# Kernel tuning notes

Measured on AMD Instinct MI355X. Metric: run time of the kernel, lower is better.

## Reference

```python
import jax, jax.numpy as jnp
import numpy as np

N_NODES = 100000
N_EDGES = 1600000
N_GRAPHS = 2000
F_IN = 16
HEADS = 8
C = 16            # per-head out channels (hidden_dim)
HC = HEADS * C    # 128
N_CLASSES = 2
NEG_SLOPE = 0.2   # PyG GATConv default leaky_relu slope


def setup_inputs() -> dict:
    key = jax.random.key(0)
    ks = jax.random.split(key, 12)
    x = jax.random.normal(ks[0], (N_NODES, F_IN), dtype=jnp.float32)
    edge_index = jax.random.randint(ks[1], (2, N_EDGES), 0, N_NODES, dtype=jnp.int32)
    batch = jnp.sort(jax.random.randint(ks[2], (N_NODES,), 0, N_GRAPHS, dtype=jnp.int32))
    s1 = 1.0 / np.sqrt(F_IN)
    s2 = 1.0 / np.sqrt(HC)
    return {
        "x": x,
        "edge_index": edge_index,
        "batch": batch,
        "W1": jax.random.normal(ks[3], (F_IN, HC), dtype=jnp.float32) * s1,
        "a1_src": jax.random.normal(ks[4], (HEADS, C), dtype=jnp.float32) * s2,
        "a1_dst": jax.random.normal(ks[5], (HEADS, C), dtype=jnp.float32) * s2,
        "b1": jnp.zeros((HC,), dtype=jnp.float32),
        "W2": jax.random.normal(ks[6], (HC, HC), dtype=jnp.float32) * s2,
        "a2_src": jax.random.normal(ks[7], (HEADS, C), dtype=jnp.float32) * s2,
        "a2_dst": jax.random.normal(ks[8], (HEADS, C), dtype=jnp.float32) * s2,
        "b2": jnp.zeros((HC,), dtype=jnp.float32),
        "lin_W": jax.random.normal(ks[9], (HC, N_CLASSES), dtype=jnp.float32) * s2,
        "lin_b": jnp.zeros((N_CLASSES,), dtype=jnp.float32),
    }


def gat_layer(h_in, src, dst, W, a_src, a_dst, b, num_nodes):
    # h: [N, H, C] per-head transformed features
    h = (h_in @ W).reshape(num_nodes, HEADS, C)
    # per-node attention half-logits: [N, H]
    logit_src = jnp.einsum('nhc,hc->nh', h, a_src)
    logit_dst = jnp.einsum('nhc,hc->nh', h, a_dst)
    # per-edge logits [E, H]
    e = jax.nn.leaky_relu(logit_src[src] + logit_dst[dst], NEG_SLOPE)
    # segment softmax over incoming edges of each destination node
    m = jax.ops.segment_max(e, dst, num_segments=num_nodes)
    m = jnp.where(jnp.isfinite(m), m, 0.0)
    ex = jnp.exp(e - m[dst])
    denom = jax.ops.segment_sum(ex, dst, num_segments=num_nodes)
    alpha = ex / jnp.maximum(denom[dst], 1e-16)
    # weighted scatter-add aggregation: [N, H, C]
    out = jax.ops.segment_sum(alpha[:, :, None] * h[src], dst, num_segments=num_nodes)
    return out.reshape(num_nodes, HC) + b


def reference(x, edge_index, batch, W1, a1_src, a1_dst, b1, W2, a2_src, a2_dst, b2, lin_W, lin_b):
    n = x.shape[0]
    # PyG GATConv adds self-loops by default
    loops = jnp.arange(n, dtype=edge_index.dtype)
    src = jnp.concatenate([edge_index[0], loops])
    dst = jnp.concatenate([edge_index[1], loops])
    h = jax.nn.relu(gat_layer(x, src, dst, W1, a1_src, a1_dst, b1, n))
    h = jax.nn.relu(gat_layer(h, src, dst, W2, a2_src, a2_dst, b2, n))
    # global mean pool per graph
    sums = jax.ops.segment_sum(h, batch, num_segments=N_GRAPHS)
    counts = jax.ops.segment_sum(jnp.ones((n, 1), h.dtype), batch, num_segments=N_GRAPHS)
    pooled = sums / jnp.maximum(counts, 1.0)
    logits = pooled @ lin_W + lin_b
    return jax.nn.softmax(logits, axis=1)
```

## Files before the change

### kernel.cpp

```cpp
#include <hip/hip_runtime.h>
#include <math.h>

#define N_NODES 100000
#define N_EDGESI 1600000
#define E_TOTAL (N_EDGESI + N_NODES)
#define N_GRAPHS 2000
#define F_IN 16
#define HEADS 8
#define CPH 16
#define HC 128
#define NEG 0.2f

#define BSHIFT 9
#define BNODES (1<<BSHIFT)
#define NBUK ((N_NODES + BNODES - 1)/BNODES)
#define BCAP 12288
#define BIN_EPT 32
#define BIN_TPB 256
#define BIN_EPB (BIN_EPT*BIN_TPB)
#define NBIN_BLK ((E_TOTAL + BIN_EPB - 1)/BIN_EPB)

#define GOFF_BLK ((N_NODES+255)/256)
#define WCONV_BLK ((HC*HC)/256)
#define XCONV_BLK ((N_NODES*4 + 255)/256)
#define W1CONV_BLK ((HC*32)/256)

typedef __bf16 bf16x8 __attribute__((ext_vector_type(8)));
typedef float  f32x4  __attribute__((ext_vector_type(4)));

__device__ __forceinline__ float leaky(float x){ return fmaxf(x, NEG*x); }
__device__ __forceinline__ float bf2f(unsigned short u){ return __uint_as_float(((unsigned)u)<<16); }
__device__ __forceinline__ unsigned short f2bf(float f){
  unsigned u = __float_as_uint(f);
  unsigned r = (u + 0x7fffu + ((u>>16)&1u)) >> 16;
  return (unsigned short)r;
}
__device__ __forceinline__ float blo(unsigned u){ return __uint_as_float(u<<16); }
__device__ __forceinline__ float bhi(unsigned u){ return __uint_as_float(u & 0xffff0000u); }

__global__ void k_pre(const int* __restrict__ ei, int* __restrict__ gpos, unsigned* __restrict__ gbin,
                      const int* __restrict__ batch, int* __restrict__ goff,
                      const float* __restrict__ W2, unsigned short* __restrict__ w2t,
                      const float* __restrict__ x, unsigned short* __restrict__ xbf,
                      const float* __restrict__ W1, unsigned short* __restrict__ w1t){
  int blk = blockIdx.x;
  if (blk < NBIN_BLK){
    __shared__ int cnt[NBUK];
    __shared__ int rnk[NBUK];
    __shared__ int bbase[NBUK];
    int t = threadIdx.x;
    for (int i = t; i < NBUK; i += BIN_TPB){ cnt[i] = 0; rnk[i] = 0; }
    __syncthreads();
    int base = blk*BIN_EPB;
    #pragma unroll 4
    for (int i = 0; i < BIN_EPT; ++i){
      int e = base + i*BIN_TPB + t;
      if (e < E_TOTAL){
        unsigned d = (e < N_EDGESI) ? (unsigned)ei[N_EDGESI + e] : (unsigned)(e - N_EDGESI);
        atomicAdd(&cnt[d >> BSHIFT], 1);
      }
    }
    __syncthreads();
    for (int i = t; i < NBUK; i += BIN_TPB){
      int v = cnt[i];
      bbase[i] = v ? atomicAdd(&gpos[i], v) : 0;
    }
    __syncthreads();
    #pragma unroll 4
    for (int i = 0; i < BIN_EPT; ++i){
      int e = base + i*BIN_TPB + t;
      if (e < E_TOTAL){
        unsigned s, d;
        if (e < N_EDGESI){ s = (unsigned)ei[e]; d = (unsigned)ei[N_EDGESI + e]; }
        else { s = d = (unsigned)(e - N_EDGESI); }
        int b = (int)(d >> BSHIFT);
        int r = atomicAdd(&rnk[b], 1);
        gbin[(size_t)b*BCAP + bbase[b] + r] = ((d & (BNODES-1u)) << 17) | s;
      }
    }
  } else if (blk < NBIN_BLK + GOFF_BLK){
    int n = (blk - NBIN_BLK)*256 + threadIdx.x;
    if (n >= N_NODES) return;
    int b = batch[n];
    if (n == 0){ for (int g = 0; g <= b; ++g) goff[g] = 0; }
    int b1 = (n+1 < N_NODES) ? batch[n+1] : N_GRAPHS;
    for (int g = b+1; g <= b1; ++g) goff[g] = n+1;
  } else if (blk < NBIN_BLK + GOFF_BLK + WCONV_BLK){
    int i = (blk - NBIN_BLK - GOFF_BLK)*256 + threadIdx.x;
    if (i >= HC*HC) return;
    int c = i >> 7, k = i & 127;
    w2t[i] = f2bf(W2[k*HC + c]);
  } else if (blk < NBIN_BLK + GOFF_BLK + WCONV_BLK + XCONV_BLK){
    int p = (blk - NBIN_BLK - GOFF_BLK - WCONV_BLK)*256 + threadIdx.x;
    if (p >= N_NODES*4) return;
    int n = p >> 2, q = p & 3;
    float4 xv = ((const float4*)(x + n*F_IN))[q];
    ushort4 o; o.x = f2bf(xv.x); o.y = f2bf(xv.y); o.z = f2bf(xv.z); o.w = f2bf(xv.w);
    ((ushort4*)(xbf + (size_t)n*32))[q] = o;
    ushort4 z; z.x = 0; z.y = 0; z.z = 0; z.w = 0;
    ((ushort4*)(xbf + (size_t)n*32 + 16))[q] = z;
  } else {
    int i = (blk - NBIN_BLK - GOFF_BLK - WCONV_BLK - XCONV_BLK)*256 + threadIdx.x;
    if (i >= HC*32) return;
    int c = i >> 5, k = i & 31;
    w1t[i] = (k < F_IN) ? f2bf(W1[k*HC + c]) : (unsigned short)0;
  }
}

__global__ __launch_bounds__(512) void k_csr(
                      const int* __restrict__ gpos, const unsigned* __restrict__ gbin,
                      int* __restrict__ off, int* __restrict__ csrc){
  __shared__ int lcnt[BNODES];
  __shared__ int wsum[8];
  __shared__ int gp[NBUK];
  __shared__ int sbase;
  int b = blockIdx.x, t = threadIdx.x;
  for (int i = t; i < NBUK; i += 512) gp[i] = gpos[i];
  lcnt[t] = 0;
  __syncthreads();
  if (t == 0){ int s = 0; for (int j = 0; j < b; ++j) s += gp[j]; sbase = s; }
  int nb = gp[b];
  const unsigned* bb = gbin + (size_t)b*BCAP;
  __syncthreads();
  int base = sbase;
  for (int i = t; i < nb; i += 512) atomicAdd(&lcnt[bb[i] >> 17], 1);
  __syncthreads();
  int lane = t & 63, wv = t >> 6;
  int v = lcnt[t];
  int sc = v;
  #pragma unroll
  for (int o = 1; o < 64; o <<= 1){ int u = __shfl_up(sc, o, 64); if (lane >= o) sc += u; }
  if (lane == 63) wsum[wv] = sc;
  __syncthreads();
  if (wv == 0 && lane < 8){
    int w2 = wsum[lane];
    #pragma unroll
    for (int o = 1; o < 8; o <<= 1){ int u = __shfl_up(w2, o, 64); if (lane >= o) w2 += u; }
    wsum[lane] = w2;
  }
  __syncthreads();
  int excl = (wv ? wsum[wv-1] : 0) + sc - v;
  int d = (b << BSHIFT) + t;
  if (d < N_NODES) off[d] = base + excl;
  if (b == NBUK-1 && t == 0) off[N_NODES] = E_TOTAL;
  __syncthreads();
  lcnt[t] = base + excl;
  __syncthreads();
  for (int i = t; i < nb; i += 512){
    unsigned en = bb[i];
    int p = atomicAdd(&lcnt[en >> 17], 1);
    csrc[p] = (int)(en & 0x1ffffu);
  }
}

template<int KS>
__global__ __launch_bounds__(256) void k_gemm_mfma(
                             const unsigned short* __restrict__ hin,
                             const unsigned short* __restrict__ wt,
                             const float* __restrict__ asrc, const float* __restrict__ adst,
                             unsigned short* __restrict__ hb,
                             float* __restrict__ ls, float* __restrict__ ld){
  __shared__ unsigned short hls[64][132];
  const int KST = KS*32;
  int t = threadIdx.x, lane = t & 63, wv = t >> 6;
  int n0 = blockIdx.x*64 + wv*16;
  int rowl = lane & 15, kgrp = lane >> 4;
  int row = n0 + rowl;
  int rowc = (row < N_NODES) ? row : (N_NODES-1);
  bf16x8 a[KS];
  #pragma unroll
  for (int ks = 0; ks < KS; ++ks)
    a[ks] = *(const bf16x8*)(hin + (size_t)rowc*KST + ks*32 + kgrp*8);
  #pragma unroll
  for (int ct = 0; ct < 8; ++ct){
    f32x4 acc = {0.f, 0.f, 0.f, 0.f};
    int col = ct*16 + rowl;
    #pragma unroll
    for (int ks = 0; ks < KS; ++ks){
      bf16x8 b = *(const bf16x8*)(wt + (size_t)col*KST + ks*32 + kgrp*8);
      acc = __builtin_amdgcn_mfma_f32_16x16x32_bf16(a[ks], b, acc, 0, 0, 0);
    }
    #pragma unroll
    for (int r = 0; r < 4; ++r){
      int lrow = wv*16 + kgrp*4 + r;
      int ro = n0 + kgrp*4 + r;
      unsigned short hv = f2bf(acc[r]);
      hls[lrow][col] = hv;
      if (ro < N_NODES) hb[(size_t)ro*HC + col] = hv;
    }
  }
  __syncthreads();
  #pragma unroll
  for (int pp = 0; pp < 2; ++pp){
    int p = t + pp*256;
    int lrow = p >> 3, h = p & 7;
    int gn = blockIdx.x*64 + lrow;
    if (gn < N_NODES){
      const unsigned short* rp = &hls[lrow][h*16];
      uint2 A = *(const uint2*)rp;
      uint2 B = *(const uint2*)(rp+4);
      uint2 C = *(const uint2*)(rp+8);
      uint2 D = *(const uint2*)(rp+12);
      float c[16] = { blo(A.x), bhi(A.x), blo(A.y), bhi(A.y),
                      blo(B.x), bhi(B.x), blo(B.y), bhi(B.y),
                      blo(C.x), bhi(C.x), blo(C.y), bhi(C.y),
                      blo(D.x), bhi(D.x), blo(D.y), bhi(D.y) };
      const float* as = asrc + h*CPH;
      const float* ad = adst + h*CPH;
      float s0 = 0.f, s1 = 0.f;
      #pragma unroll
      for (int q = 0; q < 16; ++q){ s0 += c[q]*as[q]; s1 += c[q]*ad[q]; }
      ls[gn*8 + h] = s0;
      ld[gn*8 + h] = s1;
    }
  }
}

__global__ void k_agg(const int* __restrict__ off, const int* __restrict__ csrc,
                      const unsigned short* __restrict__ hb, const float* __restrict__ ls,
                      const float* __restrict__ ld, const float* __restrict__ bias,
                      unsigned short* __restrict__ outb){
  int wid = threadIdx.x >> 6, lane = threadIdx.x & 63;
  int n = blockIdx.x*4 + wid;
  if (n >= N_NODES) return;
  int rs = __builtin_amdgcn_readfirstlane(off[n]);
  int re = __builtin_amdgcn_readfirstlane(off[n+1]);
  int q = lane >> 4;
  int l = lane & 15;
  int h = l >> 1;
  float ldh = ld[n*8 + h];
  const uint4* hb4 = (const uint4*)hb;
  float ac0=0.f, ac1=0.f, ac2=0.f, ac3=0.f, ac4=0.f, ac5=0.f, ac6=0.f, ac7=0.f, dsum=0.f;
  #define AGG_BODY(J) { \
    int s = __shfl(sv, (J), 64); \
    float g = ls[s*8 + h]; \
    float ex = __expf(leaky(g + ldh)); \
    uint4 v = hb4[(size_t)s*16 + l]; \
    ac0 += ex*blo(v.x); ac1 += ex*bhi(v.x); \
    ac2 += ex*blo(v.y); ac3 += ex*bhi(v.y); \
    ac4 += ex*blo(v.z); ac5 += ex*bhi(v.z); \
    ac6 += ex*blo(v.w); ac7 += ex*bhi(v.w); \
    dsum += ex; }
  int nb = re - rs;
  for (int cb = 0; cb < nb; cb += 64){
    int cnt = nb - cb; if (cnt > 64) cnt = 64;
    int sv = csrc[rs + cb + (lane < cnt ? lane : 0)];
    int jj = 0;
    for (; jj + 16 <= cnt; jj += 16){
      AGG_BODY(jj+q) AGG_BODY(jj+q+4) AGG_BODY(jj+q+8) AGG_BODY(jj+q+12)
    }
    for (int j = jj + q; j < cnt; j += 4) AGG_BODY(j)
  }
  #undef AGG_BODY
  ac0 += __shfl_xor(ac0,16,64); ac0 += __shfl_xor(ac0,32,64);
  ac1 += __shfl_xor(ac1,16,64); ac1 += __shfl_xor(ac1,32,64);
  ac2 += __shfl_xor(ac2,16,64); ac2 += __shfl_xor(ac2,32,64);
  ac3 += __shfl_xor(ac3,16,64); ac3 += __shfl_xor(ac3,32,64);
  ac4 += __shfl_xor(ac4,16,64); ac4 += __shfl_xor(ac4,32,64);
  ac5 += __shfl_xor(ac5,16,64); ac5 += __shfl_xor(ac5,32,64);
  ac6 += __shfl_xor(ac6,16,64); ac6 += __shfl_xor(ac6,32,64);
  ac7 += __shfl_xor(ac7,16,64); ac7 += __shfl_xor(ac7,32,64);
  dsum += __shfl_xor(dsum,16,64); dsum += __shfl_xor(dsum,32,64);
  if (q == 0){
    float inv = 1.f/fmaxf(dsum, 1e-16f);
    float4 b0 = ((const float4*)bias)[l*2];
    float4 b1 = ((const float4*)bias)[l*2+1];
    uint4 o;
    o.x = (unsigned)f2bf(fmaxf(ac0*inv + b0.x, 0.f)) | ((unsigned)f2bf(fmaxf(ac1*inv + b0.y, 0.f)) << 16);
    o.y = (unsigned)f2bf(fmaxf(ac2*inv + b0.z, 0.f)) | ((unsigned)f2bf(fmaxf(ac3*inv + b0.w, 0.f)) << 16);
    o.z = (unsigned)f2bf(fmaxf(ac4*inv + b1.x, 0.f)) | ((unsigned)f2bf(fmaxf(ac5*inv + b1.y, 0.f)) << 16);
    o.w = (unsigned)f2bf(fmaxf(ac6*inv + b1.z, 0.f)) | ((unsigned)f2bf(fmaxf(ac7*inv + b1.w, 0.f)) << 16);
    ((uint4*)outb)[(size_t)n*16 + l] = o;
  }
}

__global__ void k_poolcls(const unsigned short* __restrict__ h, const int* __restrict__ goff,
                          const float* __restrict__ lw, const float* __restrict__ lb,
                          float* __restrict__ out){
  __shared__ float sh[4][HC];
  int g = blockIdx.x;
  int t = threadIdx.x, lane = t & 63, wv = t >> 6;
  int s = goff[g], epos = goff[g+1];
  float a0 = 0.f, a1 = 0.f;
  const ushort2* h2 = (const ushort2*)h;
  for (int n = s + wv; n < epos; n += 4){
    ushort2 v = h2[(size_t)n*64 + lane];
    a0 += bf2f(v.x); a1 += bf2f(v.y);
  }
  sh[wv][lane*2] = a0; sh[wv][lane*2+1] = a1;
  __syncthreads();
  if (wv == 0){
    int c0 = lane*2;
    float p0 = sh[0][c0] + sh[1][c0] + sh[2][c0] + sh[3][c0];
    float p1 = sh[0][c0+1] + sh[1][c0+1] + sh[2][c0+1] + sh[3][c0+1];
    int cntg = epos - s;
    float invc = 1.f/fmaxf((float)cntg, 1.f);
    float v0 = p0*invc, v1 = p1*invc;
    float l0 = v0*lw[c0*2+0] + v1*lw[(c0+1)*2+0];
    float l1 = v0*lw[c0*2+1] + v1*lw[(c0+1)*2+1];
    #pragma unroll
    for (int o = 32; o >= 1; o >>= 1){ l0 += __shfl_xor(l0,o,64); l1 += __shfl_xor(l1,o,64); }
    if (lane == 0){
      l0 += lb[0]; l1 += lb[1];
      float m = fmaxf(l0,l1);
      float e0 = __expf(l0-m), e1 = __expf(l1-m);
      float si = e0 + e1;
      out[g*2]   = e0/si;
      out[g*2+1] = e1/si;
    }
  }
}

extern "C" void kernel_launch(void* const* d_in, const int* in_sizes, int n_in,
                              void* d_out, int out_size, void* d_ws, size_t ws_size,
                              hipStream_t stream){
  const float* x   = (const float*)d_in[0];
  const int*   ei  = (const int*)d_in[1];
  const int*   bat = (const int*)d_in[2];
  const float* W1  = (const float*)d_in[3];
  const float* a1s = (const float*)d_in[4];
  const float* a1d = (const float*)d_in[5];
  const float* b1  = (const float*)d_in[6];
  const float* W2  = (const float*)d_in[7];
  const float* a2s = (const float*)d_in[8];
  const float* a2d = (const float*)d_in[9];
  const float* b2  = (const float*)d_in[10];
  const float* lw  = (const float*)d_in[11];
  const float* lb  = (const float*)d_in[12];
  float* out = (float*)d_out;

  char* w = (char*)d_ws;
  auto alloc = [&](size_t bytes)->void*{ void* p = (void*)w; w += (bytes + 511) & ~size_t(511); return p; };
  int* off    = (int*)alloc((size_t)(N_NODES+1)*4);
  int* csrc   = (int*)alloc((size_t)E_TOTAL*4);
  int* goff   = (int*)alloc((size_t)(N_GRAPHS+1)*4);
  int* gpos   = (int*)alloc((size_t)NBUK*4);
  unsigned* gbin = (unsigned*)alloc((size_t)NBUK*BCAP*4);
  unsigned short* w2t  = (unsigned short*)alloc((size_t)HC*HC*2);
  unsigned short* w1t  = (unsigned short*)alloc((size_t)HC*32*2);
  unsigned short* xbf  = (unsigned short*)alloc((size_t)N_NODES*32*2);
  unsigned short* hbf  = (unsigned short*)alloc((size_t)N_NODES*HC*2);
  unsigned short* hbf2 = (unsigned short*)alloc((size_t)N_NODES*HC*2);
  float* lsb  = (float*)alloc((size_t)N_NODES*HEADS*4);
  float* ldb  = (float*)alloc((size_t)N_NODES*HEADS*4);

  hipMemsetAsync(gpos, 0, (size_t)NBUK*4, stream);

  k_pre  <<<NBIN_BLK + GOFF_BLK + WCONV_BLK + XCONV_BLK + W1CONV_BLK,BIN_TPB,0,stream>>>(
           ei, gpos, gbin, bat, goff, W2, w2t, x, xbf, W1, w1t);
  k_gemm_mfma<1><<<(N_NODES+63)/64,256,0,stream>>>(xbf, w1t, a1s, a1d, hbf, lsb, ldb);
  k_csr  <<<NBUK,512,0,stream>>>(gpos, gbin, off, csrc);

  k_agg  <<<(N_NODES+3)/4,256,0,stream>>>(off, csrc, hbf, lsb, ldb, b1, hbf2);
  k_gemm_mfma<4><<<(N_NODES+63)/64,256,0,stream>>>(hbf2, w2t, a2s, a2d, hbf, lsb, ldb);
  k_agg  <<<(N_NODES+3)/4,256,0,stream>>>(off, csrc, hbf, lsb, ldb, b2, hbf2);

  k_poolcls<<<N_GRAPHS,256,0,stream>>>(hbf2, goff, lw, lb, out);
}
```

Measured before the change: 274.9 us.

## Replace per-bucket CSR build with global degree scan and split scatter

New measurement: 371.1 us. 35.0% more time.

```diff
diff --git a/kernel.cpp b/kernel.cpp
--- a/kernel.cpp
+++ b/kernel.cpp
@@ -10,6 +10,8 @@
 #define CPH 16
 #define HC 128
 #define NEG 0.2f
+#define SCAN_B 1024
+#define NB_SCAN ((N_NODES + SCAN_B - 1)/SCAN_B)
 
 #define BSHIFT 9
 #define BNODES (1<<BSHIFT)
@@ -19,6 +21,7 @@
 #define BIN_TPB 256
 #define BIN_EPB (BIN_EPT*BIN_TPB)
 #define NBIN_BLK ((E_TOTAL + BIN_EPB - 1)/BIN_EPB)
+#define CSR_SPLIT 8
 
 #define GOFF_BLK ((N_NODES+255)/256)
 #define WCONV_BLK ((HC*HC)/256)
@@ -39,6 +42,7 @@
 __device__ __forceinline__ float bhi(unsigned u){ return __uint_as_float(u & 0xffff0000u); }
 
 __global__ void k_pre(const int* __restrict__ ei, int* __restrict__ gpos, unsigned* __restrict__ gbin,
+                      int* __restrict__ cnt_g,
                       const int* __restrict__ batch, int* __restrict__ goff,
                       const float* __restrict__ W2, unsigned short* __restrict__ w2t,
                       const float* __restrict__ x, unsigned short* __restrict__ xbf,
@@ -58,6 +62,7 @@
       if (e < E_TOTAL){
         unsigned d = (e < N_EDGESI) ? (unsigned)ei[N_EDGESI + e] : (unsigned)(e - N_EDGESI);
         atomicAdd(&cnt[d >> BSHIFT], 1);
+        atomicAdd(&cnt_g[d], 1);
       }
     }
     __syncthreads();
@@ -107,48 +112,72 @@
   }
 }
 
-__global__ __launch_bounds__(512) void k_csr(
-                      const int* __restrict__ gpos, const unsigned* __restrict__ gbin,
-                      int* __restrict__ off, int* __restrict__ csrc){
-  __shared__ int lcnt[BNODES];
-  __shared__ int wsum[8];
-  __shared__ int gp[NBUK];
-  __shared__ int sbase;
-  int b = blockIdx.x, t = threadIdx.x;
-  for (int i = t; i < NBUK; i += 512) gp[i] = gpos[i];
-  lcnt[t] = 0;
-  __syncthreads();
-  if (t == 0){ int s = 0; for (int j = 0; j < b; ++j) s += gp[j]; sbase = s; }
-  int nb = gp[b];
+__global__ void k_scan1(const int* __restrict__ cnt, int* __restrict__ off, int* __restrict__ bsum){
+  __shared__ int ws[16];
+  int b = blockIdx.x, t = threadIdx.x, lane = t & 63, wv = t >> 6;
+  int i = b*SCAN_B + t;
+  int v = (i < N_NODES) ? cnt[i] : 0;
+  int sc = v;
+  #pragma unroll
+  for (int o=1;o<64;o<<=1){ int u = __shfl_up(sc, o, 64); if (lane >= o) sc += u; }
+  if (lane==63) ws[wv] = sc;
+  __syncthreads();
+  if (wv==0 && lane<16){
+    int w = ws[lane];
+    #pragma unroll
+    for (int o=1;o<16;o<<=1){ int u = __shfl_up(w,o,64); if (lane>=o) w += u; }
+    ws[lane] = w;
+  }
+  __syncthreads();
+  int base = wv ? ws[wv-1] : 0;
+  if (i < N_NODES) off[i] = base + sc - v;
+  if (t == SCAN_B-1) bsum[b] = ws[15];
+}
+
+__global__ void k_scan2(int* __restrict__ bsum, int nb){
+  __shared__ int ws[4];
+  int t = threadIdx.x, lane = t & 63, wv = t >> 6;
+  int v = (t < nb) ? bsum[t] : 0;
+  int sc = v;
+  #pragma unroll
+  for (int o=1;o<64;o<<=1){ int u = __shfl_up(sc,o,64); if (lane>=o) sc += u; }
+  if (lane==63) ws[wv] = sc;
+  __syncthreads();
+  if (wv==0 && lane<4){
+    int w = ws[lane];
+    #pragma unroll
+    for (int o=1;o<4;o<<=1){ int u = __shfl_up(w,o,64); if (lane>=o) w += u; }
+    ws[lane] = w;
+  }
+  __syncthreads();
+  int base = wv ? ws[wv-1] : 0;
+  int excl = base + sc - v;
+  int total = ws[3];
+  __syncthreads();
+  if (t < nb) bsum[t] = excl;
+  if (t == nb) bsum[nb] = total;
+}
+
+__global__ void k_scan3(int* __restrict__ off, const int* __restrict__ bsum, int* __restrict__ cur){
+  int i = blockIdx.x*256 + threadIdx.x;
+  if (i < N_NODES){
+    int v = off[i] + bsum[i>>10];
+    off[i] = v; cur[i] = v;
+  }
+  if (i == 0) off[N_NODES] = bsum[NB_SCAN];
+}
+
+__global__ void k_csrs(const int* __restrict__ gpos, const unsigned* __restrict__ gbin,
+                       int* __restrict__ cur, int* __restrict__ csrc){
+  int b = blockIdx.x / CSR_SPLIT, part = blockIdx.x % CSR_SPLIT;
+  int nb = gpos[b];
+  int lo = (int)(((long long)nb*part)/CSR_SPLIT);
+  int hi = (int)(((long long)nb*(part+1))/CSR_SPLIT);
   const unsigned* bb = gbin + (size_t)b*BCAP;
-  __syncthreads();
-  int base = sbase;
-  for (int i = t; i < nb; i += 512) atomicAdd(&lcnt[bb[i] >> 17], 1);
-  __syncthreads();
-  int lane = t & 63, wv = t >> 6;
-  int v = lcnt[t];
-  int sc = v;
-  #pragma unroll
-  for (int o = 1; o < 64; o <<= 1){ int u = __shfl_up(sc, o, 64); if (lane >= o) sc += u; }
-  if (lane == 63) wsum[wv] = sc;
-  __syncthreads();
-  if (wv == 0 && lane < 8){
-    int w2 = wsum[lane];
-    #pragma unroll
-    for (int o = 1; o < 8; o <<= 1){ int u = __shfl_up(w2, o, 64); if (lane >= o) w2 += u; }
-    wsum[lane] = w2;
-  }
-  __syncthreads();
-  int excl = (wv ? wsum[wv-1] : 0) + sc - v;
-  int d = (b << BSHIFT) + t;
-  if (d < N_NODES) off[d] = base + excl;
-  if (b == NBUK-1 && t == 0) off[N_NODES] = E_TOTAL;
-  __syncthreads();
-  lcnt[t] = base + excl;
-  __syncthreads();
-  for (int i = t; i < nb; i += 512){
+  int d0 = b << BSHIFT;
+  for (int i = lo + threadIdx.x; i < hi; i += 256){
     unsigned en = bb[i];
-    int p = atomicAdd(&lcnt[en >> 17], 1);
+    int p = atomicAdd(&cur[d0 + (int)(en >> 17)], 1);
     csrc[p] = (int)(en & 0x1ffffu);
   }
 }
@@ -332,9 +361,12 @@
   char* w = (char*)d_ws;
   auto alloc = [&](size_t bytes)->void*{ void* p = (void*)w; w += (bytes + 511) & ~size_t(511); return p; };
   int* off    = (int*)alloc((size_t)(N_NODES+1)*4);
+  int* cur    = (int*)alloc((size_t)N_NODES*4);
+  int* cnt    = (int*)alloc((size_t)N_NODES*4);
   int* csrc   = (int*)alloc((size_t)E_TOTAL*4);
   int* goff   = (int*)alloc((size_t)(N_GRAPHS+1)*4);
   int* gpos   = (int*)alloc((size_t)NBUK*4);
+  int* bsum   = (int*)alloc((size_t)(NB_SCAN+1)*4);
   unsigned* gbin = (unsigned*)alloc((size_t)NBUK*BCAP*4);
   unsigned short* w2t  = (unsigned short*)alloc((size_t)HC*HC*2);
   unsigned short* w1t  = (unsigned short*)alloc((size_t)HC*32*2);
@@ -345,11 +377,15 @@
   float* ldb  = (float*)alloc((size_t)N_NODES*HEADS*4);
 
   hipMemsetAsync(gpos, 0, (size_t)NBUK*4, stream);
+  hipMemsetAsync(cnt, 0, (size_t)N_NODES*4, stream);
 
   k_pre  <<<NBIN_BLK + GOFF_BLK + WCONV_BLK + XCONV_BLK + W1CONV_BLK,BIN_TPB,0,stream>>>(
-           ei, gpos, gbin, bat, goff, W2, w2t, x, xbf, W1, w1t);
+           ei, gpos, gbin, cnt, bat, goff, W2, w2t, x, xbf, W1, w1t);
+  k_scan1<<<NB_SCAN,SCAN_B,0,stream>>>(cnt, off, bsum);
+  k_scan2<<<1,256,0,stream>>>(bsum, NB_SCAN);
+  k_scan3<<<(N_NODES+255)/256,256,0,stream>>>(off, bsum, cur);
   k_gemm_mfma<1><<<(N_NODES+63)/64,256,0,stream>>>(xbf, w1t, a1s, a1d, hbf, lsb, ldb);
-  k_csr  <<<NBUK,512,0,stream>>>(gpos, gbin, off, csrc);
+  k_csrs <<<NBUK*CSR_SPLIT,256,0,stream>>>(gpos, gbin, cur, csrc);
 
   k_agg  <<<(N_NODES+3)/4,256,0,stream>>>(off, csrc, hbf, lsb, ldb, b1, hbf2);
   k_gemm_mfma<4><<<(N_NODES+63)/64,256,0,stream>>>(hbf2, w2t, a2s, a2d, hbf, lsb, ldb);
```
